# Kernel optimization log

Hardware: AMD Instinct MI355X
Metric: run time of the kernel (lower is better)

## Reference

```python
import jax, jax.numpy as jnp
import numpy as np

N, D, NUM_CLASSES = 4096, 1024, 1000


def setup_inputs() -> dict:
    key = jax.random.key(0)
    k1, k2 = jax.random.split(key)
    output = jax.random.normal(k1, (N, D), dtype=jnp.float32)
    target = jax.random.randint(k2, (N,), 0, NUM_CLASSES, dtype=jnp.int64)
    return {"output": output, "target": target}


def reference(output, target):
    # k1: strictly-lower-triangular part of the gram matrix [N, N]
    gram = output @ output.T
    k1 = jnp.tril(gram, -1)
    # k2: strictly-lower-triangular label-equality mask (vectorized form of
    # the original O(N^2) python double loop)
    eq = (target[:, None] == target[None, :]).astype(output.dtype)
    k2 = jnp.tril(eq, -1)
    return -(jnp.sum(k1 * k2) / (jnp.sum(k2) * jnp.linalg.norm(k1)))
```

## Files before the change

### kernel.cpp

```cpp
#include <hip/hip_runtime.h>
#include <hip/hip_bf16.h>


typedef __attribute__((ext_vector_type(8))) short short8;
typedef __attribute__((ext_vector_type(4))) float f32x4;

#define N_ROWS 4096
#define D_DIM  1024
#define N_CLS  1000
#define NTIL   136

__device__ __forceinline__ unsigned short f2bf(float f) {
  unsigned u = __float_as_uint(f);
  u += 0x7fffu + ((u >> 16) & 1u);
  return (unsigned short)(u >> 16);
}

__device__ __forceinline__ void gload16(const short* g, const char* l) {
  __builtin_amdgcn_global_load_lds(
      (const __attribute__((address_space(1))) unsigned*)g,
      (__attribute__((address_space(3))) unsigned*)(void*)l, 16, 0, 0);
}

__global__ void __launch_bounds__(256) kconv(const float* __restrict__ A,
                                             short* __restrict__ Ab,
                                             double* __restrict__ rowp) {
  __shared__ double wr2[4];
  const int tid = threadIdx.x, lane = tid & 63, w = tid >> 6;
  const int row0 = blockIdx.x * 8;
  double ls = 0.0;
#pragma unroll
  for (int rr = 0; rr < 2; ++rr) {
    const int i = row0 + w * 2 + rr;
    const float4* src = (const float4*)(A + (size_t)i * D_DIM);
    short4* dst = (short4*)(Ab + (size_t)i * D_DIM);
    float s = 0.f;
#pragma unroll
    for (int c = 0; c < 4; ++c) {
      const float4 v = src[lane + c * 64];
      s += v.x * v.x + v.y * v.y + v.z * v.z + v.w * v.w;
      short4 o;
      o.x = (short)f2bf(v.x); o.y = (short)f2bf(v.y);
      o.z = (short)f2bf(v.z); o.w = (short)f2bf(v.w);
      dst[lane + c * 64] = o;
    }
#pragma unroll
    for (int off = 32; off; off >>= 1) s += __shfl_down(s, off);
    if (lane == 0) ls += (double)s;
  }
  if (lane == 0) wr2[w] = ls;
  __syncthreads();
  if (tid == 0) rowp[blockIdx.x] = wr2[0] + wr2[1] + wr2[2] + wr2[3];
}

__global__ void __launch_bounds__(512, 2) kmain(const float* __restrict__ A,
                                                const int* __restrict__ target,
                                                const short* __restrict__ Ab,
                                                double* __restrict__ frobp,
                                                double* __restrict__ cssp,
                                                int* __restrict__ cntp) {
  __shared__ __align__(16) char smem[131072];
  const int tid = threadIdx.x, lane = tid & 63, w = tid >> 6;

  if (blockIdx.x < NTIL) {
    const int b = (blockIdx.x & 7) * 17 + (blockIdx.x >> 3);
    int bi = (int)((sqrtf(8.f * (float)b + 1.f) - 1.f) * 0.5f);
    while ((bi + 1) * (bi + 2) / 2 <= b) ++bi;
    while (bi * (bi + 1) / 2 > b) --bi;
    const int bj = b - bi * (bi + 1) / 2;
    const bool diag = (bi == bj);

    const short* Pa = Ab + (size_t)(bi * 256) * D_DIM;
    const short* Pb = Ab + (size_t)(bj * 256) * D_DIM;

    short* As0 = (short*)smem;
    short* As1 = (short*)(smem + 32768);
    short* Bs0 = (short*)(smem + 65536);
    short* Bs1 = (short*)(smem + 98304);

    f32x4 acc[8][4];
#pragma unroll
    for (int m = 0; m < 8; ++m)
#pragma unroll
      for (int n = 0; n < 4; ++n) acc[m][n] = (f32x4){0.f, 0.f, 0.f, 0.f};

    const int wm = w >> 2, wn = w & 3;
    const int row16 = lane & 15, ck = lane >> 4;

    const int sr = tid >> 2;
    const int scS = (tid & 3) ^ ((sr >> 1) & 3);

#define STAGEU(P, BUF, h, kt)                                               \
    do {                                                                    \
      const short* _g = (P) + ((size_t)((h) * 128 + sr)) * D_DIM + (kt) * 64 + scS * 8; \
      gload16(_g,      (const char*)(BUF) + (h) * 8192 + w * 1024);         \
      gload16(_g + 32, (const char*)(BUF) + 16384 + (h) * 8192 + w * 1024); \
    } while (0)

#define RD_A(BUF, MH)                                                       \
    _Pragma("unroll") for (int ks = 0; ks < 2; ++ks)                        \
    _Pragma("unroll") for (int m = 0; m < 4; ++m) {                         \
      const int R = wm * 128 + ((MH) * 4 + m) * 16 + row16;                 \
      a[ks][m] = *(const short8*)((const char*)(BUF) + ks * 16384 + R * 64  \
                                  + ((ck ^ ((R >> 1) & 3)) << 4));          \
    }
#define RD_B(DST, BUF, NH)                                                  \
    _Pragma("unroll") for (int ks = 0; ks < 2; ++ks)                        \
    _Pragma("unroll") for (int n = 0; n < 2; ++n) {                         \
      const int R = wn * 64 + ((NH) * 2 + n) * 16 + row16;                  \
      DST[ks][n] = *(const short8*)((const char*)(BUF) + ks * 16384 + R * 64\
                                    + ((ck ^ ((R >> 1) & 3)) << 4));        \
    }
#define PH_MFMA(MO, NO, BB)                                                 \
    __builtin_amdgcn_s_setprio(1);                                          \
    _Pragma("unroll") for (int ks = 0; ks < 2; ++ks)                        \
    _Pragma("unroll") for (int m = 0; m < 4; ++m)                           \
    _Pragma("unroll") for (int n = 0; n < 2; ++n)                           \
      acc[(MO) + m][(NO) + n] = __builtin_amdgcn_mfma_f32_16x16x32_bf16(    \
          a[ks][m], BB[ks][n], acc[(MO) + m][(NO) + n], 0, 0, 0);           \
    __builtin_amdgcn_s_setprio(0);
#define BAR __builtin_amdgcn_s_barrier()
#define VM0 asm volatile("s_waitcnt vmcnt(0)" ::: "memory")

    STAGEU(Pa, As0, 0, 0); STAGEU(Pa, As0, 1, 0);
    STAGEU(Pb, Bs0, 0, 0); STAGEU(Pb, Bs0, 1, 0);
    VM0;
    BAR;

#pragma unroll 1
    for (int it = 0; it < 8; ++it) {
      const int t1 = 2 * it + 1, t2 = 2 * it + 2;
      short8 a[2][4], bq0[2][2], b[2][2];
      RD_A(As0, 0); RD_B(bq0, Bs0, 0);
      STAGEU(Pa, As1, 0, t1); STAGEU(Pa, As1, 1, t1);
      BAR;
      PH_MFMA(0, 0, bq0);
      BAR;
      RD_B(b, Bs0, 1);
      STAGEU(Pb, Bs1, 0, t1); STAGEU(Pb, Bs1, 1, t1);
      BAR;
      PH_MFMA(0, 2, b);
      BAR;
      RD_A(As0, 1);
      BAR;
      PH_MFMA(4, 2, b);
      BAR;
      PH_MFMA(4, 0, bq0);
      BAR;
      VM0;
      BAR;
      RD_A(As1, 0); RD_B(bq0, Bs1, 0);
      if (it < 7) { STAGEU(Pa, As0, 0, t2); STAGEU(Pa, As0, 1, t2); }
      BAR;
      PH_MFMA(0, 0, bq0);
      BAR;
      RD_B(b, Bs1, 1);
      if (it < 7) { STAGEU(Pb, Bs0, 0, t2); STAGEU(Pb, Bs0, 1, t2); }
      BAR;
      PH_MFMA(0, 2, b);
      BAR;
      RD_A(As1, 1);
      BAR;
      PH_MFMA(4, 2, b);
      BAR;
      PH_MFMA(4, 0, bq0);
      BAR;
      VM0;
      BAR;
    }
#undef STAGEU
#undef RD_A
#undef RD_B
#undef PH_MFMA
#undef BAR
#undef VM0

    float fs = 0.f;
    if (!diag) {
#pragma unroll
      for (int m = 0; m < 8; ++m)
#pragma unroll
        for (int n = 0; n < 4; ++n)
#pragma unroll
          for (int q = 0; q < 4; ++q) fs += acc[m][n][q] * acc[m][n][q];
    } else {
      const int rbase = (lane >> 4) * 4, cbase = lane & 15;
#pragma unroll
      for (int m = 0; m < 8; ++m)
#pragma unroll
        for (int n = 0; n < 4; ++n)
#pragma unroll
          for (int q = 0; q < 4; ++q) {
            const int rl = wm * 128 + m * 16 + rbase + q;
            const int cl = wn * 64 + n * 16 + cbase;
            if (rl > cl) fs += acc[m][n][q] * acc[m][n][q];
          }
    }
#pragma unroll
    for (int off = 32; off; off >>= 1) fs += __shfl_down(fs, off);
    double* wredd = (double*)smem;
    if (lane == 0) wredd[w] = (double)fs;
    __syncthreads();
    if (tid == 0) {
      double t = 0.0;
#pragma unroll
      for (int i = 0; i < 8; ++i) t += wredd[i];
      frobp[b] = t;
    }
  } else {
    int* list = (int*)smem;
    int* lcnt = (int*)(smem + 16384);
    float* wredf = (float*)(smem + 16400);
    const int c = blockIdx.x - NTIL;
    if (c >= N_CLS) return;
    if (tid == 0) *lcnt = 0;
    __syncthreads();
    for (int j = tid; j < N_ROWS; j += 512)
      if (target[j] == c) { int p = atomicAdd(lcnt, 1); list[p] = j; }
    __syncthreads();
    const int n = *lcnt;
    float2 acc = make_float2(0.f, 0.f);
    for (int m = 0; m < n; ++m) {
      const float2 v = *(const float2*)(A + (size_t)list[m] * D_DIM + tid * 2);
      acc.x += v.x; acc.y += v.y;
    }
    float s = acc.x * acc.x + acc.y * acc.y;
#pragma unroll
    for (int off = 32; off; off >>= 1) s += __shfl_down(s, off);
    if (lane == 0) wredf[w] = s;
    __syncthreads();
    if (tid == 0) {
      float t = 0.f;
#pragma unroll
      for (int i = 0; i < 8; ++i) t += wredf[i];
      cssp[c] = (double)t;
      cntp[c] = n;
    }
  }
}

__global__ void __launch_bounds__(256) kfinal(const double* __restrict__ rowp,
                                              const double* __restrict__ cssp,
                                              const int* __restrict__ cntp,
                                              const double* __restrict__ frobp,
                                              float* __restrict__ out) {
  __shared__ double red[256];
  const int tid = threadIdx.x;
  double lsum = rowp[tid] + rowp[tid + 256];
  double lcss = 0.0, lcnn = 0.0, lfr = 0.0;
  for (int c = tid; c < N_CLS; c += 256) {
    lcss += cssp[c];
    const double nc = (double)cntp[c];
    lcnn += nc * nc;
  }
  if (tid < NTIL) lfr = frobp[tid];

  double vals[4] = {lsum, lcss, lcnn, lfr};
  double res[4];
  for (int v = 0; v < 4; ++v) {
    red[tid] = vals[v];
    __syncthreads();
    for (int s = 128; s; s >>= 1) {
      if (tid < s) red[tid] += red[tid + s];
      __syncthreads();
    }
    res[v] = red[0];
    __syncthreads();
  }
  if (tid == 0) {
    const double sumr = res[0], css = res[1], cnn = res[2], frob = res[3];
    const double S1 = 0.5 * (css - sumr);
    const double S2 = 0.5 * (cnn - (double)N_ROWS);
    const double S3 = frob;
    out[0] = (float)(-(S1 / (S2 * sqrt(S3))));
  }
}

extern "C" void kernel_launch(void* const* d_in, const int* in_sizes, int n_in,
                              void* d_out, int out_size, void* d_ws, size_t ws_size,
                              hipStream_t stream) {
  const float* A = (const float*)d_in[0];
  const int* target = (const int*)d_in[1];
  float* out = (float*)d_out;

  char* ws = (char*)d_ws;
  short*  Ab    = (short*)ws;
  double* rowp  = (double*)(ws + 8388608);
  double* cssp  = (double*)(ws + 8388608 + 4096);
  int*    cntp  = (int*)   (ws + 8388608 + 4096 + 8000);
  double* frobp = (double*)(ws + 8388608 + 4096 + 8000 + 4096);

  kconv<<<512, 256, 0, stream>>>(A, Ab, rowp);
  kmain<<<NTIL + N_CLS, 512, 0, stream>>>(A, target, Ab, frobp, cssp, cntp);
  kfinal<<<1, 256, 0, stream>>>(rowp, cssp, cntp, frobp, out);
}
```

Before: 45.51 us.

## Move per-class sum work from gram kernel into conversion kernel

The per-class row-sum blocks now run in the bf16 conversion kernel (256 threads, float4 loads) instead of sharing a launch with the gram tiles. The gram kernel becomes a pure 136-block MFMA kernel, so its 128KB-LDS blocks no longer share the launch with the class blocks, each of which reserves the full 128KB smem array. The cost is that the prep kernel grows to 1512 blocks, and the class-sum work is no longer overlapped with the bandwidth-light gram tiles.

```diff
diff --git a/kernel.cpp b/kernel.cpp
--- a/kernel.cpp
+++ b/kernel.cpp
@@ -22,152 +22,179 @@
       (__attribute__((address_space(3))) unsigned*)(void*)l, 16, 0, 0);
 }
 
-__global__ void __launch_bounds__(256) kconv(const float* __restrict__ A,
+__global__ void __launch_bounds__(256) kprep(const float* __restrict__ A,
+                                             const int* __restrict__ target,
                                              short* __restrict__ Ab,
-                                             double* __restrict__ rowp) {
-  __shared__ double wr2[4];
+                                             double* __restrict__ rowp,
+                                             double* __restrict__ cssp,
+                                             int* __restrict__ cntp) {
   const int tid = threadIdx.x, lane = tid & 63, w = tid >> 6;
-  const int row0 = blockIdx.x * 8;
-  double ls = 0.0;
-#pragma unroll
-  for (int rr = 0; rr < 2; ++rr) {
-    const int i = row0 + w * 2 + rr;
-    const float4* src = (const float4*)(A + (size_t)i * D_DIM);
-    short4* dst = (short4*)(Ab + (size_t)i * D_DIM);
-    float s = 0.f;
-#pragma unroll
-    for (int c = 0; c < 4; ++c) {
-      const float4 v = src[lane + c * 64];
-      s += v.x * v.x + v.y * v.y + v.z * v.z + v.w * v.w;
-      short4 o;
-      o.x = (short)f2bf(v.x); o.y = (short)f2bf(v.y);
-      o.z = (short)f2bf(v.z); o.w = (short)f2bf(v.w);
-      dst[lane + c * 64] = o;
-    }
+
+  if (blockIdx.x < 512) {
+    __shared__ double wr2[4];
+    const int row0 = blockIdx.x * 8;
+    double ls = 0.0;
+#pragma unroll
+    for (int rr = 0; rr < 2; ++rr) {
+      const int i = row0 + w * 2 + rr;
+      const float4* src = (const float4*)(A + (size_t)i * D_DIM);
+      short4* dst = (short4*)(Ab + (size_t)i * D_DIM);
+      float s = 0.f;
+#pragma unroll
+      for (int c = 0; c < 4; ++c) {
+        const float4 v = src[lane + c * 64];
+        s += v.x * v.x + v.y * v.y + v.z * v.z + v.w * v.w;
+        short4 o;
+        o.x = (short)f2bf(v.x); o.y = (short)f2bf(v.y);
+        o.z = (short)f2bf(v.z); o.w = (short)f2bf(v.w);
+        dst[lane + c * 64] = o;
+      }
+#pragma unroll
+      for (int off = 32; off; off >>= 1) s += __shfl_down(s, off);
+      if (lane == 0) ls += (double)s;
+    }
+    if (lane == 0) wr2[w] = ls;
+    __syncthreads();
+    if (tid == 0) rowp[blockIdx.x] = wr2[0] + wr2[1] + wr2[2] + wr2[3];
+  } else {
+    __shared__ int list[N_ROWS];
+    __shared__ int lcnt;
+    __shared__ float wred[4];
+    const int c = blockIdx.x - 512;
+    if (c >= N_CLS) return;
+    if (tid == 0) lcnt = 0;
+    __syncthreads();
+    for (int j = tid; j < N_ROWS; j += 256)
+      if (target[j] == c) { int p = atomicAdd(&lcnt, 1); list[p] = j; }
+    __syncthreads();
+    const int n = lcnt;
+    float4 acc = make_float4(0.f, 0.f, 0.f, 0.f);
+    for (int m = 0; m < n; ++m) {
+      const float4 v = *(const float4*)(A + (size_t)list[m] * D_DIM + tid * 4);
+      acc.x += v.x; acc.y += v.y; acc.z += v.z; acc.w += v.w;
+    }
+    float s = acc.x * acc.x + acc.y * acc.y + acc.z * acc.z + acc.w * acc.w;
 #pragma unroll
     for (int off = 32; off; off >>= 1) s += __shfl_down(s, off);
-    if (lane == 0) ls += (double)s;
-  }
-  if (lane == 0) wr2[w] = ls;
-  __syncthreads();
-  if (tid == 0) rowp[blockIdx.x] = wr2[0] + wr2[1] + wr2[2] + wr2[3];
-}
-
-__global__ void __launch_bounds__(512, 2) kmain(const float* __restrict__ A,
-                                                const int* __restrict__ target,
-                                                const short* __restrict__ Ab,
-                                                double* __restrict__ frobp,
-                                                double* __restrict__ cssp,
-                                                int* __restrict__ cntp) {
+    if (lane == 0) wred[w] = s;
+    __syncthreads();
+    if (tid == 0) {
+      cssp[c] = (double)(wred[0] + wred[1] + wred[2] + wred[3]);
+      cntp[c] = n;
+    }
+  }
+}
+
+__global__ void __launch_bounds__(512, 2) kgram(const short* __restrict__ Ab,
+                                                double* __restrict__ frobp) {
   __shared__ __align__(16) char smem[131072];
   const int tid = threadIdx.x, lane = tid & 63, w = tid >> 6;
 
-  if (blockIdx.x < NTIL) {
-    const int b = (blockIdx.x & 7) * 17 + (blockIdx.x >> 3);
-    int bi = (int)((sqrtf(8.f * (float)b + 1.f) - 1.f) * 0.5f);
-    while ((bi + 1) * (bi + 2) / 2 <= b) ++bi;
-    while (bi * (bi + 1) / 2 > b) --bi;
-    const int bj = b - bi * (bi + 1) / 2;
-    const bool diag = (bi == bj);
-
-    const short* Pa = Ab + (size_t)(bi * 256) * D_DIM;
-    const short* Pb = Ab + (size_t)(bj * 256) * D_DIM;
-
-    short* As0 = (short*)smem;
-    short* As1 = (short*)(smem + 32768);
-    short* Bs0 = (short*)(smem + 65536);
-    short* Bs1 = (short*)(smem + 98304);
-
-    f32x4 acc[8][4];
-#pragma unroll
-    for (int m = 0; m < 8; ++m)
-#pragma unroll
-      for (int n = 0; n < 4; ++n) acc[m][n] = (f32x4){0.f, 0.f, 0.f, 0.f};
-
-    const int wm = w >> 2, wn = w & 3;
-    const int row16 = lane & 15, ck = lane >> 4;
-
-    const int sr = tid >> 2;
-    const int scS = (tid & 3) ^ ((sr >> 1) & 3);
+  const int b = (blockIdx.x & 7) * 17 + (blockIdx.x >> 3);
+  int bi = (int)((sqrtf(8.f * (float)b + 1.f) - 1.f) * 0.5f);
+  while ((bi + 1) * (bi + 2) / 2 <= b) ++bi;
+  while (bi * (bi + 1) / 2 > b) --bi;
+  const int bj = b - bi * (bi + 1) / 2;
+  const bool diag = (bi == bj);
+
+  const short* Pa = Ab + (size_t)(bi * 256) * D_DIM;
+  const short* Pb = Ab + (size_t)(bj * 256) * D_DIM;
+
+  short* As0 = (short*)smem;
+  short* As1 = (short*)(smem + 32768);
+  short* Bs0 = (short*)(smem + 65536);
+  short* Bs1 = (short*)(smem + 98304);
+
+  f32x4 acc[8][4];
+#pragma unroll
+  for (int m = 0; m < 8; ++m)
+#pragma unroll
+    for (int n = 0; n < 4; ++n) acc[m][n] = (f32x4){0.f, 0.f, 0.f, 0.f};
+
+  const int wm = w >> 2, wn = w & 3;
+  const int row16 = lane & 15, ck = lane >> 4;
+
+  const int sr = tid >> 2;
+  const int scS = (tid & 3) ^ ((sr >> 1) & 3);
 
 #define STAGEU(P, BUF, h, kt)                                               \
-    do {                                                                    \
-      const short* _g = (P) + ((size_t)((h) * 128 + sr)) * D_DIM + (kt) * 64 + scS * 8; \
-      gload16(_g,      (const char*)(BUF) + (h) * 8192 + w * 1024);         \
-      gload16(_g + 32, (const char*)(BUF) + 16384 + (h) * 8192 + w * 1024); \
-    } while (0)
+  do {                                                                      \
+    const short* _g = (P) + ((size_t)((h) * 128 + sr)) * D_DIM + (kt) * 64 + scS * 8; \
+    gload16(_g,      (const char*)(BUF) + (h) * 8192 + w * 1024);           \
+    gload16(_g + 32, (const char*)(BUF) + 16384 + (h) * 8192 + w * 1024);   \
+  } while (0)
 
 #define RD_A(BUF, MH)                                                       \
-    _Pragma("unroll") for (int ks = 0; ks < 2; ++ks)                        \
-    _Pragma("unroll") for (int m = 0; m < 4; ++m) {                         \
-      const int R = wm * 128 + ((MH) * 4 + m) * 16 + row16;                 \
-      a[ks][m] = *(const short8*)((const char*)(BUF) + ks * 16384 + R * 64  \
+  _Pragma("unroll") for (int ks = 0; ks < 2; ++ks)                          \
+  _Pragma("unroll") for (int m = 0; m < 4; ++m) {                           \
+    const int R = wm * 128 + ((MH) * 4 + m) * 16 + row16;                   \
+    a[ks][m] = *(const short8*)((const char*)(BUF) + ks * 16384 + R * 64    \
+                                + ((ck ^ ((R >> 1) & 3)) << 4));            \
+  }
+#define RD_B(DST, BUF, NH)                                                  \
+  _Pragma("unroll") for (int ks = 0; ks < 2; ++ks)                          \
+  _Pragma("unroll") for (int n = 0; n < 2; ++n) {                           \
+    const int R = wn * 64 + ((NH) * 2 + n) * 16 + row16;                    \
+    DST[ks][n] = *(const short8*)((const char*)(BUF) + ks * 16384 + R * 64  \
                                   + ((ck ^ ((R >> 1) & 3)) << 4));          \
-    }
-#define RD_B(DST, BUF, NH)                                                  \
-    _Pragma("unroll") for (int ks = 0; ks < 2; ++ks)                        \
-    _Pragma("unroll") for (int n = 0; n < 2; ++n) {                         \
-      const int R = wn * 64 + ((NH) * 2 + n) * 16 + row16;                  \
-      DST[ks][n] = *(const short8*)((const char*)(BUF) + ks * 16384 + R * 64\
-                                    + ((ck ^ ((R >> 1) & 3)) << 4));        \
-    }
+  }
 #define PH_MFMA(MO, NO, BB)                                                 \
-    __builtin_amdgcn_s_setprio(1);                                          \
-    _Pragma("unroll") for (int ks = 0; ks < 2; ++ks)                        \
-    _Pragma("unroll") for (int m = 0; m < 4; ++m)                           \
-    _Pragma("unroll") for (int n = 0; n < 2; ++n)                           \
-      acc[(MO) + m][(NO) + n] = __builtin_amdgcn_mfma_f32_16x16x32_bf16(    \
-          a[ks][m], BB[ks][n], acc[(MO) + m][(NO) + n], 0, 0, 0);           \
-    __builtin_amdgcn_s_setprio(0);
+  __builtin_amdgcn_s_setprio(1);                                            \
+  _Pragma("unroll") for (int ks = 0; ks < 2; ++ks)                          \
+  _Pragma("unroll") for (int m = 0; m < 4; ++m)                             \
+  _Pragma("unroll") for (int n = 0; n < 2; ++n)                             \
+    acc[(MO) + m][(NO) + n] = __builtin_amdgcn_mfma_f32_16x16x32_bf16(      \
+        a[ks][m], BB[ks][n], acc[(MO) + m][(NO) + n], 0, 0, 0);             \
+  __builtin_amdgcn_s_setprio(0);
 #define BAR __builtin_amdgcn_s_barrier()
 #define VM0 asm volatile("s_waitcnt vmcnt(0)" ::: "memory")
 
-    STAGEU(Pa, As0, 0, 0); STAGEU(Pa, As0, 1, 0);
-    STAGEU(Pb, Bs0, 0, 0); STAGEU(Pb, Bs0, 1, 0);
+  STAGEU(Pa, As0, 0, 0); STAGEU(Pa, As0, 1, 0);
+  STAGEU(Pb, Bs0, 0, 0); STAGEU(Pb, Bs0, 1, 0);
+  VM0;
+  BAR;
+
+#pragma unroll 1
+  for (int it = 0; it < 8; ++it) {
+    const int t1 = 2 * it + 1, t2 = 2 * it + 2;
+    short8 a[2][4], bq0[2][2], b[2][2];
+    RD_A(As0, 0); RD_B(bq0, Bs0, 0);
+    STAGEU(Pa, As1, 0, t1); STAGEU(Pa, As1, 1, t1);
+    BAR;
+    PH_MFMA(0, 0, bq0);
+    BAR;
+    RD_B(b, Bs0, 1);
+    STAGEU(Pb, Bs1, 0, t1); STAGEU(Pb, Bs1, 1, t1);
+    BAR;
+    PH_MFMA(0, 2, b);
+    BAR;
+    RD_A(As0, 1);
+    BAR;
+    PH_MFMA(4, 2, b);
+    BAR;
+    PH_MFMA(4, 0, bq0);
+    BAR;
     VM0;
     BAR;
-
-#pragma unroll 1
-    for (int it = 0; it < 8; ++it) {
-      const int t1 = 2 * it + 1, t2 = 2 * it + 2;
-      short8 a[2][4], bq0[2][2], b[2][2];
-      RD_A(As0, 0); RD_B(bq0, Bs0, 0);
-      STAGEU(Pa, As1, 0, t1); STAGEU(Pa, As1, 1, t1);
-      BAR;
-      PH_MFMA(0, 0, bq0);
-      BAR;
-      RD_B(b, Bs0, 1);
-      STAGEU(Pb, Bs1, 0, t1); STAGEU(Pb, Bs1, 1, t1);
-      BAR;
-      PH_MFMA(0, 2, b);
-      BAR;
-      RD_A(As0, 1);
-      BAR;
-      PH_MFMA(4, 2, b);
-      BAR;
-      PH_MFMA(4, 0, bq0);
-      BAR;
-      VM0;
-      BAR;
-      RD_A(As1, 0); RD_B(bq0, Bs1, 0);
-      if (it < 7) { STAGEU(Pa, As0, 0, t2); STAGEU(Pa, As0, 1, t2); }
-      BAR;
-      PH_MFMA(0, 0, bq0);
-      BAR;
-      RD_B(b, Bs1, 1);
-      if (it < 7) { STAGEU(Pb, Bs0, 0, t2); STAGEU(Pb, Bs0, 1, t2); }
-      BAR;
-      PH_MFMA(0, 2, b);
-      BAR;
-      RD_A(As1, 1);
-      BAR;
-      PH_MFMA(4, 2, b);
-      BAR;
-      PH_MFMA(4, 0, bq0);
-      BAR;
-      VM0;
-      BAR;
-    }
+    RD_A(As1, 0); RD_B(bq0, Bs1, 0);
+    if (it < 7) { STAGEU(Pa, As0, 0, t2); STAGEU(Pa, As0, 1, t2); }
+    BAR;
+    PH_MFMA(0, 0, bq0);
+    BAR;
+    RD_B(b, Bs1, 1);
+    if (it < 7) { STAGEU(Pb, Bs0, 0, t2); STAGEU(Pb, Bs0, 1, t2); }
+    BAR;
+    PH_MFMA(0, 2, b);
+    BAR;
+    RD_A(As1, 1);
+    BAR;
+    PH_MFMA(4, 2, b);
+    BAR;
+    PH_MFMA(4, 0, bq0);
+    BAR;
+    VM0;
+    BAR;
+  }
 #undef STAGEU
 #undef RD_A
 #undef RD_B
@@ -175,67 +202,38 @@
 #undef BAR
 #undef VM0
 
-    float fs = 0.f;
-    if (!diag) {
-#pragma unroll
-      for (int m = 0; m < 8; ++m)
-#pragma unroll
-        for (int n = 0; n < 4; ++n)
-#pragma unroll
-          for (int q = 0; q < 4; ++q) fs += acc[m][n][q] * acc[m][n][q];
-    } else {
-      const int rbase = (lane >> 4) * 4, cbase = lane & 15;
-#pragma unroll
-      for (int m = 0; m < 8; ++m)
-#pragma unroll
-        for (int n = 0; n < 4; ++n)
-#pragma unroll
-          for (int q = 0; q < 4; ++q) {
-            const int rl = wm * 128 + m * 16 + rbase + q;
-            const int cl = wn * 64 + n * 16 + cbase;
-            if (rl > cl) fs += acc[m][n][q] * acc[m][n][q];
-          }
-    }
-#pragma unroll
-    for (int off = 32; off; off >>= 1) fs += __shfl_down(fs, off);
-    double* wredd = (double*)smem;
-    if (lane == 0) wredd[w] = (double)fs;
-    __syncthreads();
-    if (tid == 0) {
-      double t = 0.0;
-#pragma unroll
-      for (int i = 0; i < 8; ++i) t += wredd[i];
-      frobp[b] = t;
-    }
+  float fs = 0.f;
+  if (!diag) {
+#pragma unroll
+    for (int m = 0; m < 8; ++m)
+#pragma unroll
+      for (int n = 0; n < 4; ++n)
+#pragma unroll
+        for (int q = 0; q < 4; ++q) fs += acc[m][n][q] * acc[m][n][q];
   } else {
-    int* list = (int*)smem;
-    int* lcnt = (int*)(smem + 16384);
-    float* wredf = (float*)(smem + 16400);
-    const int c = blockIdx.x - NTIL;
-    if (c >= N_CLS) return;
-    if (tid == 0) *lcnt = 0;
-    __syncthreads();
-    for (int j = tid; j < N_ROWS; j += 512)
-      if (target[j] == c) { int p = atomicAdd(lcnt, 1); list[p] = j; }
-    __syncthreads();
-    const int n = *lcnt;
-    float2 acc = make_float2(0.f, 0.f);
-    for (int m = 0; m < n; ++m) {
-      const float2 v = *(const float2*)(A + (size_t)list[m] * D_DIM + tid * 2);
-      acc.x += v.x; acc.y += v.y;
-    }
-    float s = acc.x * acc.x + acc.y * acc.y;
-#pragma unroll
-    for (int off = 32; off; off >>= 1) s += __shfl_down(s, off);
-    if (lane == 0) wredf[w] = s;
-    __syncthreads();
-    if (tid == 0) {
-      float t = 0.f;
-#pragma unroll
-      for (int i = 0; i < 8; ++i) t += wredf[i];
-      cssp[c] = (double)t;
-      cntp[c] = n;
-    }
+    const int rbase = (lane >> 4) * 4, cbase = lane & 15;
+#pragma unroll
+    for (int m = 0; m < 8; ++m)
+#pragma unroll
+      for (int n = 0; n < 4; ++n)
+#pragma unroll
+        for (int q = 0; q < 4; ++q) {
+          const int rl = wm * 128 + m * 16 + rbase + q;
+          const int cl = wn * 64 + n * 16 + cbase;
+          if (rl > cl) fs += acc[m][n][q] * acc[m][n][q];
+        }
+  }
+#pragma unroll
+  for (int off = 32; off; off >>= 1) fs += __shfl_down(fs, off);
+  double* wredd = (double*)smem;
+  __syncthreads();
+  if (lane == 0) wredd[w] = (double)fs;
+  __syncthreads();
+  if (tid == 0) {
+    double t = 0.0;
+#pragma unroll
+    for (int i = 0; i < 8; ++i) t += wredd[i];
+    frobp[b] = t;
   }
 }
 
@@ -290,7 +288,7 @@
   int*    cntp  = (int*)   (ws + 8388608 + 4096 + 8000);
   double* frobp = (double*)(ws + 8388608 + 4096 + 8000 + 4096);
 
-  kconv<<<512, 256, 0, stream>>>(A, Ab, rowp);
-  kmain<<<NTIL + N_CLS, 512, 0, stream>>>(A, target, Ab, frobp, cssp, cntp);
+  kprep<<<512 + N_CLS, 256, 0, stream>>>(A, target, Ab, rowp, cssp, cntp);
+  kgram<<<NTIL, 512, 0, stream>>>(Ab, frobp);
   kfinal<<<1, 256, 0, stream>>>(rowp, cssp, cntp, frobp, out);
 }
```

Result: slower. 49.26 us (+8.3%).

## Prefetch two K-tiles ahead with partial vmcnt waits in gram GEMM

Applied to the files above, without the earlier changes.

Restructures the double-buffered bf16 GEMM main loop so each iteration issues the global-to-LDS loads for tile t+2 into the buffer just consumed, then waits with vmcnt(8) rather than draining all outstanding loads. This keeps one tile of loads in flight across iterations and removes the full vmcnt(0) drain plus several barriers per tile, aiming to hide memory latency behind the MFMA phases. It adds a sched_barrier to stop the compiler reordering around the waits, and a __syncthreads before the reduction scratch write, which now reuses LDS that may still hold tile data.

```diff
diff --git a/kernel.cpp b/kernel.cpp
--- a/kernel.cpp
+++ b/kernel.cpp
@@ -9,6 +9,7 @@
 #define D_DIM  1024
 #define N_CLS  1000
 #define NTIL   136
+#define NKT    16
 
 __device__ __forceinline__ unsigned short f2bf(float f) {
   unsigned u = __float_as_uint(f);
@@ -73,10 +74,10 @@
     const short* Pa = Ab + (size_t)(bi * 256) * D_DIM;
     const short* Pb = Ab + (size_t)(bj * 256) * D_DIM;
 
-    short* As0 = (short*)smem;
-    short* As1 = (short*)(smem + 32768);
-    short* Bs0 = (short*)(smem + 65536);
-    short* Bs1 = (short*)(smem + 98304);
+    short* const As0 = (short*)smem;
+    short* const As1 = (short*)(smem + 32768);
+    short* const Bs0 = (short*)(smem + 65536);
+    short* const Bs1 = (short*)(smem + 98304);
 
     f32x4 acc[8][4];
 #pragma unroll
@@ -95,6 +96,12 @@
       const short* _g = (P) + ((size_t)((h) * 128 + sr)) * D_DIM + (kt) * 64 + scS * 8; \
       gload16(_g,      (const char*)(BUF) + (h) * 8192 + w * 1024);         \
       gload16(_g + 32, (const char*)(BUF) + 16384 + (h) * 8192 + w * 1024); \
+    } while (0)
+
+#define STAGET(AB, BB, kt)                                                  \
+    do {                                                                    \
+      STAGEU(Pa, AB, 0, kt); STAGEU(Pa, AB, 1, kt);                         \
+      STAGEU(Pb, BB, 0, kt); STAGEU(Pb, BB, 1, kt);                         \
     } while (0)
 
 #define RD_A(BUF, MH)                                                       \
@@ -120,60 +127,49 @@
           a[ks][m], BB[ks][n], acc[(MO) + m][(NO) + n], 0, 0, 0);           \
     __builtin_amdgcn_s_setprio(0);
 #define BAR __builtin_amdgcn_s_barrier()
-#define VM0 asm volatile("s_waitcnt vmcnt(0)" ::: "memory")
-
-    STAGEU(Pa, As0, 0, 0); STAGEU(Pa, As0, 1, 0);
-    STAGEU(Pb, Bs0, 0, 0); STAGEU(Pb, Bs0, 1, 0);
-    VM0;
+#define SBZ __builtin_amdgcn_sched_barrier(0)
+
+    STAGET(As0, Bs0, 0);
+    asm volatile("s_waitcnt vmcnt(0)" ::: "memory");
+    SBZ;
     BAR;
+    STAGET(As1, Bs1, 1);
 
 #pragma unroll 1
-    for (int it = 0; it < 8; ++it) {
-      const int t1 = 2 * it + 1, t2 = 2 * it + 2;
-      short8 a[2][4], bq0[2][2], b[2][2];
-      RD_A(As0, 0); RD_B(bq0, Bs0, 0);
-      STAGEU(Pa, As1, 0, t1); STAGEU(Pa, As1, 1, t1);
+    for (int t = 0; t < NKT; ++t) {
+      const int c = t & 1;
+      short* const As = c ? As1 : As0;
+      short* const Bs = c ? Bs1 : Bs0;
+      short8 a[2][4], bq0[2][2], b1[2][2];
+      RD_A(As, 0); RD_B(bq0, Bs, 0);
       BAR;
       PH_MFMA(0, 0, bq0);
       BAR;
-      RD_B(b, Bs0, 1);
-      STAGEU(Pb, Bs1, 0, t1); STAGEU(Pb, Bs1, 1, t1);
-      BAR;
-      PH_MFMA(0, 2, b);
-      BAR;
-      RD_A(As0, 1);
-      BAR;
-      PH_MFMA(4, 2, b);
-      BAR;
+      RD_B(b1, Bs, 1);
+      BAR;
+      PH_MFMA(0, 2, b1);
+      BAR;
+      RD_A(As, 1);
+      BAR;
+      PH_MFMA(4, 2, b1);
+      BAR;
+      if (t + 2 < NKT) STAGET(As, Bs, t + 2);
       PH_MFMA(4, 0, bq0);
-      BAR;
-      VM0;
-      BAR;
-      RD_A(As1, 0); RD_B(bq0, Bs1, 0);
-      if (it < 7) { STAGEU(Pa, As0, 0, t2); STAGEU(Pa, As0, 1, t2); }
-      BAR;
-      PH_MFMA(0, 0, bq0);
-      BAR;
-      RD_B(b, Bs1, 1);
-      if (it < 7) { STAGEU(Pb, Bs0, 0, t2); STAGEU(Pb, Bs0, 1, t2); }
-      BAR;
-      PH_MFMA(0, 2, b);
-      BAR;
-      RD_A(As1, 1);
-      BAR;
-      PH_MFMA(4, 2, b);
-      BAR;
-      PH_MFMA(4, 0, bq0);
-      BAR;
-      VM0;
+      if (t + 2 < NKT) {
+        asm volatile("s_waitcnt vmcnt(8)" ::: "memory");
+      } else if (t + 1 < NKT) {
+        asm volatile("s_waitcnt vmcnt(0)" ::: "memory");
+      }
+      SBZ;
       BAR;
     }
 #undef STAGEU
+#undef STAGET
 #undef RD_A
 #undef RD_B
 #undef PH_MFMA
 #undef BAR
-#undef VM0
+#undef SBZ
 
     float fs = 0.f;
     if (!diag) {
@@ -199,6 +195,7 @@
 #pragma unroll
     for (int off = 32; off; off >>= 1) fs += __shfl_down(fs, off);
     double* wredd = (double*)smem;
+    __syncthreads();
     if (lane == 0) wredd[w] = (double)fs;
     __syncthreads();
     if (tid == 0) {
```

Measured after the change: 46.99 us. 3.3% more time.
